# Performance work log

Hardware: AMD Instinct MI355X
Metric: run time of the kernel (lower is better)

Reference implementation:

```python
import jax, jax.numpy as jnp
import numpy as np

B, W, CBLK, C, H, L, VOCAB = 8, 512, 24, 512, 8, 2, 256
HD = C // H


def _ln(x, g, b, eps=1e-5):
    m = x.mean(-1, keepdims=True)
    v = ((x - m) ** 2).mean(-1, keepdims=True)
    return (x - m) * jax.lax.rsqrt(v + eps) * g + b


def _causal_attn(q, k, v):
    # q,k,v: [..., T, hd]; causal softmax attention, scale 1/sqrt(hd)
    T = q.shape[-2]
    scale = 1.0 / (q.shape[-1] ** 0.5)
    s = jnp.einsum('...qd,...kd->...qk', q, k) * scale
    mask = jnp.tril(jnp.ones((T, T), dtype=bool))
    s = jnp.where(mask, s, jnp.finfo(s.dtype).min)
    return jnp.einsum('...qk,...kd->...qd', jax.nn.softmax(s, axis=-1), v)


def _mha_char(seq, w_qkv, last_ix):
    # seq: [B,W,c,C]; per-word causal char attention, then gather row last_ix
    b, w, c, _ = seq.shape
    q, k, v = jnp.split(seq @ w_qkv, 3, axis=-1)
    sh = lambda t: t.reshape(b, w, c, H, HD).transpose(0, 1, 3, 2, 4)
    o = _causal_attn(sh(q), sh(k), sh(v))          # [B,W,H,c,hd]
    o = o.transpose(0, 1, 3, 2, 4).reshape(b, w, c, C)
    return jnp.take_along_axis(o, last_ix[:, :, None, None], axis=2)[:, :, 0, :]


def _mha_word(x, w_qkv, w_proj):
    b, w, _ = x.shape
    q, k, v = jnp.split(x @ w_qkv, 3, axis=-1)
    sh = lambda t: t.reshape(b, w, H, HD).transpose(0, 2, 1, 3)
    o = _causal_attn(sh(q), sh(k), sh(v))
    o = o.transpose(0, 2, 1, 3).reshape(b, w, C)
    return o @ w_proj


def setup_inputs() -> dict:
    key = jax.random.key(0)
    ks = jax.random.split(key, 16)
    # ragged word lengths in [1, CBLK]; mask = ones then zeros (as produced by pad())
    lengths = jax.random.randint(ks[0], (B, W), 1, CBLK + 1)
    attention_mask = (jnp.arange(CBLK)[None, None, :] < lengths[:, :, None]).astype(jnp.int32)
    x = jax.random.randint(ks[1], (B, W, CBLK), 0, VOCAB).astype(jnp.int32)
    std = 0.02
    res_std = std * (2 * L) ** -0.5  # res_flag init scaling
    n = lambda k, s, sd=std: sd * jax.random.normal(k, s, dtype=jnp.float32)
    return dict(
        x=x, attention_mask=attention_mask,
        cte=n(ks[2], (VOCAB, C)), cpe=n(ks[3], (CBLK, C)), wpe=n(ks[4], (W, C)),
        ln1_g=jnp.ones((L, C)), ln1_b=jnp.zeros((L, C)),
        ln2_g=jnp.ones((L, C)), ln2_b=jnp.zeros((L, C)),
        ln3_g=jnp.ones((L, C)), ln3_b=jnp.zeros((L, C)),
        cattn_w=n(ks[5], (L, C, 3 * C)), cattn_proj=n(ks[6], (L, C, C)),
        wattn_w=n(ks[7], (L, C, 3 * C)), wattn_proj=n(ks[8], (L, C, C), res_std),
        mlp_fc=n(ks[9], (L, C, 4 * C)), mlp_proj=n(ks[10], (L, 4 * C, C), res_std),
        proj_w=n(ks[11], (C, CBLK * C)), lm_head_w=n(ks[12], (C, VOCAB)),
    )


def reference(x, attention_mask, cte, cpe, wpe, ln1_g, ln1_b, ln2_g, ln2_b, ln3_g, ln3_b,
              cattn_w, cattn_proj, wattn_w, wattn_proj, mlp_fc, mlp_proj, proj_w, lm_head_w):
    last_ix = attention_mask.sum(axis=2) - 1           # [B,W], last real char per word
    state = cte[x] + cpe[None, None, :, :]             # [B,W,c,C]
    context = None                                     # current_conv.context/pad, vectorized
    for l in range(L):
        if l == 0:
            # first_time: operate on full padded char sequences, cache ln_1 output
            hln = _ln(state, ln1_g[l], ln1_b[l])       # [B,W,c,C]
            context = hln
            seq = hln
        else:
            # splice the new word vector into position last_ix of the cached context
            hln = _ln(state, ln1_g[l], ln1_b[l])       # [B,W,C]
            repl = jnp.arange(CBLK)[None, None, :] == last_ix[:, :, None]
            seq = jnp.where(repl[..., None], hln[:, :, None, :], context)
        o = _mha_char(seq, cattn_w[l], last_ix)        # [B,W,C]
        if l == 0:
            o = o + wpe[None, :, :]                    # word pos emb added only first_time
        state = o @ cattn_proj[l]                      # note: no residual around c_attn
        state = state + _mha_word(_ln(state, ln2_g[l], ln2_b[l]), wattn_w[l], wattn_proj[l])
        hm = _ln(state, ln3_g[l], ln3_b[l])
        state = state + jax.nn.gelu(hm @ mlp_fc[l], approximate=False) @ mlp_proj[l]
    y = (state @ proj_w).reshape(B, W, CBLK, C)
    return y @ lm_head_w                               # logits [B,W,CBLK,VOCAB]
```

## Files before the change

kernel.cpp:

```cpp
#include <hip/hip_runtime.h>
#include <hip/hip_bf16.h>
#include <math.h>


namespace {

constexpr int Bn = 8, Wn = 512, CB = 24, Cd = 512, Hn = 8, Lln = 2, Vn = 256, HDn = 64;
constexpr int BW = Bn * Wn;
constexpr int C3 = 3 * Cd;
constexpr int FF = 4 * Cd;
constexpr int NROW = BW * CB;

typedef unsigned short u16;
typedef short short8 __attribute__((ext_vector_type(8)));
typedef float f32x4 __attribute__((ext_vector_type(4)));
typedef __attribute__((address_space(1))) void gvoid_t;
typedef __attribute__((address_space(3))) void lvoid_t;

__device__ __forceinline__ u16 f2bu(float f) {
  __hip_bfloat16 h = __float2bfloat16(f);
  return __builtin_bit_cast(u16, h);
}
__device__ __forceinline__ float bu2f(u16 u) {
  return __bfloat162float(__builtin_bit_cast(__hip_bfloat16, u));
}
__device__ __forceinline__ float geluf(float x) {
  return 0.5f * x * (1.0f + erff(x * 0.7071067811865475f));
}
__device__ __forceinline__ void gl16(const void* g, void* l) {
  __builtin_amdgcn_global_load_lds((gvoid_t*)g, (lvoid_t*)l, 16, 0, 0);
}

__global__ void k_lastix(const int* __restrict__ mask, int* __restrict__ lastix) {
  int i = blockIdx.x * 256 + threadIdx.x;
  if (i < BW) {
    int s = 0;
#pragma unroll
    for (int j = 0; j < CB; ++j) s += mask[i * CB + j];
    lastix[i] = s - 1;
  }
}

__device__ __forceinline__ void f2b8(const float* __restrict__ s, u16* __restrict__ d) {
  float4 a = *(const float4*)s;
  float4 b = *(const float4*)(s + 4);
  union { uint4 u; u16 h[8]; } pk;
  pk.h[0] = f2bu(a.x); pk.h[1] = f2bu(a.y); pk.h[2] = f2bu(a.z); pk.h[3] = f2bu(a.w);
  pk.h[4] = f2bu(b.x); pk.h[5] = f2bu(b.y); pk.h[6] = f2bu(b.z); pk.h[7] = f2bu(b.w);
  *(uint4*)d = pk.u;
}

__device__ __forceinline__ void wT_tile(const float* __restrict__ src, u16* __restrict__ dst,
                                        int K, int N, int n0, int k0,
                                        u16 T[64][72], int tid) {
  int kl = tid >> 2, nc = (tid & 3) * 16;
  const float* s = src + (long)(k0 + kl) * N + n0 + nc;
#pragma unroll
  for (int u = 0; u < 4; ++u) {
    float4 f = *(const float4*)(s + u * 4);
    T[nc + u * 4 + 0][kl] = f2bu(f.x);
    T[nc + u * 4 + 1][kl] = f2bu(f.y);
    T[nc + u * 4 + 2][kl] = f2bu(f.z);
    T[nc + u * 4 + 3][kl] = f2bu(f.w);
  }
  __syncthreads();
  int nl = tid >> 2, kc = (tid & 3) * 16;
  u16* d = dst + (long)(n0 + nl) * K + k0 + kc;
  *(uint4*)d = *(uint4*)&T[nl][kc];
  *(uint4*)(d + 8) = *(uint4*)&T[nl][kc + 8];
}

__global__ __launch_bounds__(256) void k_prep(
    const float* __restrict__ proj_w, u16* __restrict__ projwb,
    const float* __restrict__ cattn_w, u16* __restrict__ wcb,
    const float* __restrict__ lm_head, u16* __restrict__ lmhT,
    const float* __restrict__ cattn_proj, const float* __restrict__ wattn_w,
    const float* __restrict__ wattn_proj, const float* __restrict__ mlp_fc,
    const float* __restrict__ mlp_proj, u16* __restrict__ wT) {
  __shared__ u16 T[64][72];
  int b = blockIdx.x, tid = threadIdx.x;
  if (b < 3072) { long i = ((long)b * 256 + tid) * 8; f2b8(proj_w + i, projwb + i); return; }
  b -= 3072;
  if (b < 768) { long i = ((long)b * 256 + tid) * 8; f2b8(cattn_w + i, wcb + i); return; }
  b -= 768;
  if (b < 32) { wT_tile(lm_head, lmhT, Cd, Vn, (b & 3) * 64, (b >> 2) * 64, T, tid); return; }
  b -= 32;
  int l = b >> 10, r = b & 1023;
  size_t lw = (size_t)(2 * C3 * Cd + 2 * Cd * Cd + 2 * FF * Cd);
  u16* bl = wT + l * lw;
  const float* src; u16* dst; int K, N, nt;
  if (r < 192)      { src = cattn_w + (size_t)l * Cd * C3;    dst = bl;                              K = Cd; N = C3; nt = 24; }
  else if (r < 256) { src = cattn_proj + (size_t)l * Cd * Cd; dst = bl + C3 * Cd;                    K = Cd; N = Cd; nt = 8;  r -= 192; }
  else if (r < 448) { src = wattn_w + (size_t)l * Cd * C3;    dst = bl + C3 * Cd + Cd * Cd;          K = Cd; N = C3; nt = 24; r -= 256; }
  else if (r < 512) { src = wattn_proj + (size_t)l * Cd * Cd; dst = bl + 2 * C3 * Cd + Cd * Cd;      K = Cd; N = Cd; nt = 8;  r -= 448; }
  else if (r < 768) { src = mlp_fc + (size_t)l * Cd * FF;     dst = bl + 2 * C3 * Cd + 2 * Cd * Cd;  K = Cd; N = FF; nt = 32; r -= 512; }
  else              { src = mlp_proj + (size_t)l * FF * Cd;   dst = bl + 2 * C3 * Cd + 2 * Cd * Cd + FF * Cd; K = FF; N = Cd; nt = 8; r -= 768; }
  wT_tile(src, dst, K, N, (r % nt) * 64, (r / nt) * 64, T, tid);
}

__global__ __launch_bounds__(64) void k_embed_ln(
    const int* __restrict__ x, const float* __restrict__ cte, const float* __restrict__ cpe,
    const float* __restrict__ g, const float* __restrict__ b,
    const int* __restrict__ lastix, u16* __restrict__ ctx) {
  int r = blockIdx.x;
  int bw = r / CB, ch = r - bw * CB;
  if (ch > lastix[bw]) return;
  int tok = x[r];
  const float* e = cte + (long)tok * Cd;
  const float* pe = cpe + (long)ch * Cd;
  int lane = threadIdx.x;
  float v[8];
  float s = 0.f, sq = 0.f;
#pragma unroll
  for (int u = 0; u < 2; ++u) {
    float4 a = *(const float4*)(e + u * 256 + lane * 4);
    float4 p4 = *(const float4*)(pe + u * 256 + lane * 4);
    v[u * 4 + 0] = a.x + p4.x; v[u * 4 + 1] = a.y + p4.y;
    v[u * 4 + 2] = a.z + p4.z; v[u * 4 + 3] = a.w + p4.w;
  }
#pragma unroll
  for (int u = 0; u < 8; ++u) { s += v[u]; sq += v[u] * v[u]; }
#pragma unroll
  for (int m = 32; m; m >>= 1) { s += __shfl_xor(s, m); sq += __shfl_xor(sq, m); }
  float mean = s * (1.0f / Cd);
  float var = sq * (1.0f / Cd) - mean * mean;
  float rs = rsqrtf(var + 1e-5f);
  u16* o = ctx + (long)r * Cd;
#pragma unroll
  for (int u = 0; u < 2; ++u) {
    int c0 = u * 256 + lane * 4;
    float4 g4 = *(const float4*)(g + c0);
    float4 b4 = *(const float4*)(b + c0);
    float o0 = (v[u * 4 + 0] - mean) * rs * g4.x + b4.x;
    float o1 = (v[u * 4 + 1] - mean) * rs * g4.y + b4.y;
    float o2 = (v[u * 4 + 2] - mean) * rs * g4.z + b4.z;
    float o3 = (v[u * 4 + 3] - mean) * rs * g4.w + b4.w;
    uint2 w;
    w.x = (unsigned)f2bu(o0) | ((unsigned)f2bu(o1) << 16);
    w.y = (unsigned)f2bu(o2) | ((unsigned)f2bu(o3) << 16);
    *(uint2*)(o + c0) = w;
  }
}

__global__ __launch_bounds__(64) void k_ln(
    const float* __restrict__ X, u16* __restrict__ Y,
    const float* __restrict__ g, const float* __restrict__ b) {
  long r = blockIdx.x;
  const float* xr = X + r * Cd;
  int lane = threadIdx.x;
  float v[8];
  float s = 0.f, sq = 0.f;
#pragma unroll
  for (int u = 0; u < 2; ++u) {
    float4 a = *(const float4*)(xr + u * 256 + lane * 4);
    v[u * 4 + 0] = a.x; v[u * 4 + 1] = a.y; v[u * 4 + 2] = a.z; v[u * 4 + 3] = a.w;
  }
#pragma unroll
  for (int u = 0; u < 8; ++u) { s += v[u]; sq += v[u] * v[u]; }
#pragma unroll
  for (int m = 32; m; m >>= 1) { s += __shfl_xor(s, m); sq += __shfl_xor(sq, m); }
  float mean = s * (1.0f / Cd);
  float var = sq * (1.0f / Cd) - mean * mean;
  float rs = rsqrtf(var + 1e-5f);
  u16* o = Y + r * Cd;
#pragma unroll
  for (int u = 0; u < 2; ++u) {
    int c0 = u * 256 + lane * 4;
    float4 g4 = *(const float4*)(g + c0);
    float4 b4 = *(const float4*)(b + c0);
    float o0 = (v[u * 4 + 0] - mean) * rs * g4.x + b4.x;
    float o1 = (v[u * 4 + 1] - mean) * rs * g4.y + b4.y;
    float o2 = (v[u * 4 + 2] - mean) * rs * g4.z + b4.z;
    float o3 = (v[u * 4 + 3] - mean) * rs * g4.w + b4.w;
    uint2 w;
    w.x = (unsigned)f2bu(o0) | ((unsigned)f2bu(o1) << 16);
    w.y = (unsigned)f2bu(o2) | ((unsigned)f2bu(o3) << 16);
    *(uint2*)(o + c0) = w;
  }
}

__global__ __launch_bounds__(64) void k_gather_last(
    const u16* __restrict__ ctx, const int* __restrict__ lastix, u16* __restrict__ qin) {
  long bw = blockIdx.x;
  int r = (int)bw * CB + lastix[bw];
  const uint4* s = (const uint4*)(ctx + (long)r * Cd);
  uint4* d = (uint4*)(qin + bw * Cd);
  d[threadIdx.x] = s[threadIdx.x];
}

template <int BM, int BN, int EPI, int OUTBF>
__global__ __launch_bounds__(256) void k_mgemm(
    const u16* __restrict__ A, int lda, long sA1, long sA2,
    const u16* __restrict__ Bt, int ldb, long sB1, long sB2,
    void* __restrict__ Cv, int ldc, long sC1, long sC2,
    const float* __restrict__ R, u16* __restrict__ D2,
    const float* __restrict__ PL, const u16* __restrict__ VL,
    const float* __restrict__ WP, int K, int zdiv) {
  constexpr int WM = BM / 2;
  constexpr int WN = BN / 2;
  constexpr int FM = WM / 16, FN = WN / 16;
  __shared__ u16 As[BM * 32];
  __shared__ u16 Bs[BN * 32];
  long m0 = (long)blockIdx.y * BM, n0 = (long)blockIdx.x * BN;
  int z = blockIdx.z;
  int z1 = z / zdiv, z2 = z - z1 * zdiv;
  A += z1 * sA1 + z2 * sA2;
  Bt += z1 * sB1 + z2 * sB2;
  long coff = z1 * sC1 + z2 * sC2;
  int tid = threadIdx.x;
  int wid = tid >> 6, lane = tid & 63;
  int wr = wid >> 1, wc = wid & 1;

  const int srow = tid >> 2, skk = (tid & 3) * 8;
  const u16* Ald[BM / 64];
  const u16* Bld[BN / 64];
#pragma unroll
  for (int i = 0; i < BM / 64; ++i) Ald[i] = A + (m0 + srow + i * 64) * (long)lda + skk;
#pragma unroll
  for (int i = 0; i < BN / 64; ++i) Bld[i] = Bt + (n0 + srow + i * 64) * (long)ldb + skk;

  f32x4 acc[FM][FN] = {};
  const int fr = lane & 15, kg = lane >> 4;

  for (int k0 = 0; k0 < K; k0 += 32) {
#pragma unroll
    for (int i = 0; i < BM / 64; ++i) gl16(Ald[i] + k0, &As[(tid + i * 256) * 8]);
#pragma unroll
    for (int i = 0; i < BN / 64; ++i) gl16(Bld[i] + k0, &Bs[(tid + i * 256) * 8]);
    __syncthreads();
    short8 af[FM], bf[FN];
#pragma unroll
    for (int m = 0; m < FM; ++m)
      af[m] = *(const short8*)&As[(wr * WM + m * 16 + fr) * 32 + kg * 8];
#pragma unroll
    for (int n = 0; n < FN; ++n)
      bf[n] = *(const short8*)&Bs[(wc * WN + n * 16 + fr) * 32 + kg * 8];
#pragma unroll
    for (int m = 0; m < FM; ++m)
#pragma unroll
      for (int n = 0; n < FN; ++n)
        acc[m][n] = __builtin_amdgcn_mfma_f32_16x16x32_bf16(af[m], bf[n], acc[m][n], 0, 0, 0);
    __syncthreads();
  }
  int ccol = lane & 15, crow4 = (lane >> 4) * 4;
#pragma unroll
  for (int m = 0; m < FM; ++m)
#pragma unroll
    for (int n = 0; n < FN; ++n)
#pragma unroll
      for (int q = 0; q < 4; ++q) {
        long gr = m0 + wr * WM + m * 16 + crow4 + q;
        long gc = n0 + wc * WN + n * 16 + ccol;
        float v = acc[m][n][q];
        long idx = gr * (long)ldc + gc + coff;
        if (EPI == 1 || EPI == 3) v += R[idx];
        if (EPI == 2) v = geluf(v);
        if (EPI == 4) {
          v += PL[gr * 8 + z2] * bu2f(VL[gr * (long)C3 + 2 * Cd + z2 * 64 + gc]);
          if (WP) v += WP[(long)(gr & (Wn - 1)) * Cd + z2 * 64 + gc];
        }
        if (EPI == 3) {
          ((float*)Cv)[idx] = v;
          D2[idx] = f2bu(v);
        } else if (OUTBF) {
          ((u16*)Cv)[idx] = f2bu(v);
        } else {
          ((float*)Cv)[idx] = v;
        }
      }
}

__global__ __launch_bounds__(256) void k_cattn2(
    const u16* __restrict__ ctx, const u16* __restrict__ qtil,
    const u16* __restrict__ qkvc, const int* __restrict__ lastix,
    u16* __restrict__ U, float* __restrict__ plast) {
  int gw = blockIdx.x;
  int li = lastix[gw];
  __shared__ u16 ctxs[CB][512];
  __shared__ u16 qks[2][512];
  __shared__ float sp[Hn][CB];
  int tid = threadIdx.x;
  for (int u = tid; u < li * 64; u += 256) {
    int row = u >> 6, c = (u & 63) * 8;
    *(uint4*)&ctxs[row][c] = *(const uint4*)(ctx + ((long)(gw * CB + row)) * Cd + c);
  }
  if (tid < 128) {
    int row = tid >> 6, c = (tid & 63) * 8;
    *(uint4*)&qks[row][c] = *(const uint4*)(qkvc + (long)gw * C3 + row * 512 + c);
  }
  int wid = tid >> 6, lane = tid & 63;
  int h0 = wid * 2, h1 = h0 + 1;
  float q0[8], q1[8];
  {
    const u16* q0p = qtil + (long)gw * 4096 + h0 * 512 + lane * 8;
    uint4 a = *(const uint4*)q0p;
    uint4 b = *(const uint4*)(q0p + 512);
    const u16* qa = (const u16*)&a;
    const u16* qb = (const u16*)&b;
#pragma unroll
    for (int u = 0; u < 8; ++u) { q0[u] = bu2f(qa[u]); q1[u] = bu2f(qb[u]); }
  }
  __syncthreads();
  for (int j = 0; j < li; ++j) {
    float p0 = 0.f, p1 = 0.f;
    const u16* cv = &ctxs[j][lane * 8];
#pragma unroll
    for (int u = 0; u < 8; ++u) {
      float c = bu2f(cv[u]);
      p0 += c * q0[u];
      p1 += c * q1[u];
    }
#pragma unroll
    for (int m = 32; m; m >>= 1) { p0 += __shfl_xor(p0, m); p1 += __shfl_xor(p1, m); }
    if (lane == 0) { sp[h0][j] = p0 * 0.125f; sp[h1][j] = p1 * 0.125f; }
  }
  {
    float pr = 0.f;
    const u16* qq = &qks[0][lane * 8];
    const u16* kk = &qks[1][lane * 8];
#pragma unroll
    for (int u = 0; u < 8; ++u) pr += bu2f(qq[u]) * bu2f(kk[u]);
    float a0 = ((lane >> 3) == h0) ? pr : 0.f;
    float a1 = ((lane >> 3) == h1) ? pr : 0.f;
#pragma unroll
    for (int m = 32; m; m >>= 1) { a0 += __shfl_xor(a0, m); a1 += __shfl_xor(a1, m); }
    if (lane == 0) { sp[h0][li] = a0 * 0.125f; sp[h1][li] = a1 * 0.125f; }
  }
  __syncthreads();
  if (tid < 8) {
    float m = -3.4e38f;
    for (int j = 0; j <= li; ++j) m = fmaxf(m, sp[tid][j]);
    float s = 0.f;
    for (int j = 0; j <= li; ++j) { float e = expf(sp[tid][j] - m); sp[tid][j] = e; s += e; }
    float inv = 1.0f / s;
    for (int j = 0; j <= li; ++j) sp[tid][j] *= inv;
    plast[gw * 8 + tid] = sp[tid][li];
  }
  __syncthreads();
  int h = tid >> 5, d0 = (tid & 31) * 16;
  float uacc[16];
#pragma unroll
  for (int i = 0; i < 16; ++i) uacc[i] = 0.f;
  for (int j = 0; j < li; ++j) {
    float p = sp[h][j];
    const u16* cv = &ctxs[j][d0];
#pragma unroll
    for (int i = 0; i < 16; ++i) uacc[i] += p * bu2f(cv[i]);
  }
  union { uint4 q[2]; u16 hh[16]; } pk;
#pragma unroll
  for (int i = 0; i < 16; ++i) pk.hh[i] = f2bu(uacc[i]);
  u16* d = U + (long)gw * 4096 + h * 512 + d0;
  *(uint4*)d = pk.q[0];
  *(uint4*)(d + 8) = pk.q[1];
}

__global__ __launch_bounds__(256) void k_vt(const u16* __restrict__ qkv, u16* __restrict__ Vt) {
  __shared__ u16 T[64][72];
  int z = blockIdx.y, jt = blockIdx.x;
  int b = z >> 3, h = z & 7;
  int tid = threadIdx.x;
  int jl = tid >> 2, dc = (tid & 3) * 16;
  const u16* s = qkv + ((long)(b * Wn + jt * 64 + jl)) * C3 + 2 * Cd + h * HDn + dc;
  *(uint4*)&T[jl][dc] = *(const uint4*)s;
  *(uint4*)&T[jl][dc + 8] = *(const uint4*)(s + 8);
  __syncthreads();
  int dl = tid >> 2, jc = (tid & 3) * 16;
  u16 tmp[16];
#pragma unroll
  for (int u = 0; u < 16; ++u) tmp[u] = T[jc + u][dl];
  u16* d = Vt + (long)z * HDn * Wn + (long)dl * Wn + jt * 64 + jc;
  *(uint4*)d = *(uint4*)&tmp[0];
  *(uint4*)(d + 8) = *(uint4*)&tmp[8];
}

__global__ __launch_bounds__(64) void k_wsoftmax(const float* __restrict__ S,
                                                 u16* __restrict__ P) {
  long row = blockIdx.x;
  int i = (int)(row & (Wn - 1));
  const float* p = S + row * Wn;
  int lane = threadIdx.x;
  int j0 = lane * 8;
  float v[8];
  float4 a = *(const float4*)(p + j0);
  float4 b4 = *(const float4*)(p + j0 + 4);
  v[0] = a.x; v[1] = a.y; v[2] = a.z; v[3] = a.w;
  v[4] = b4.x; v[5] = b4.y; v[6] = b4.z; v[7] = b4.w;
  float m = -3.4e38f;
#pragma unroll
  for (int u = 0; u < 8; ++u) {
    v[u] = (j0 + u <= i) ? v[u] * 0.125f : -3.4e38f;
    m = fmaxf(m, v[u]);
  }
#pragma unroll
  for (int mk = 32; mk; mk >>= 1) m = fmaxf(m, __shfl_xor(m, mk));
  float s = 0.f;
#pragma unroll
  for (int u = 0; u < 8; ++u) {
    float e = (j0 + u <= i) ? expf(v[u] - m) : 0.f;
    v[u] = e; s += e;
  }
#pragma unroll
  for (int mk = 32; mk; mk >>= 1) s += __shfl_xor(s, mk);
  float inv = 1.0f / s;
  union { uint4 u; u16 h[8]; } pk;
#pragma unroll
  for (int u = 0; u < 8; ++u) pk.h[u] = f2bu(v[u] * inv);
  *(uint4*)(P + row * Wn + j0) = pk.u;
}

template <int BM, int BN, int EPI, int OUTBF>
static inline void mgemm(hipStream_t st,
    const u16* A, int lda, long sA1, long sA2,
    const u16* Bt, int ldb, long sB1, long sB2,
    void* C, int ldc, long sC1, long sC2,
    const float* R, int M, int N, int K, int nz, int zdiv,
    u16* D2 = nullptr, const float* PL = nullptr, const u16* VL = nullptr,
    const float* WP = nullptr) {
  dim3 g(N / BN, (M + BM - 1) / BM, nz);
  hipLaunchKernelGGL((k_mgemm<BM, BN, EPI, OUTBF>), g, dim3(256), 0, st,
                     A, lda, sA1, sA2, Bt, ldb, sB1, sB2, C, ldc, sC1, sC2,
                     R ? R : (const float*)C, D2, PL, VL, WP, K, zdiv);
}

}

extern "C" void kernel_launch(void* const* d_in, const int* in_sizes, int n_in,
                              void* d_out, int out_size, void* d_ws, size_t ws_size,
                              hipStream_t stream) {
  (void)in_sizes; (void)n_in; (void)out_size; (void)ws_size;
  const int*   x          = (const int*)d_in[0];
  const int*   amask      = (const int*)d_in[1];
  const float* cte        = (const float*)d_in[2];
  const float* cpe        = (const float*)d_in[3];
  const float* wpe        = (const float*)d_in[4];
  const float* ln1g       = (const float*)d_in[5];
  const float* ln1b       = (const float*)d_in[6];
  const float* ln2g       = (const float*)d_in[7];
  const float* ln2b       = (const float*)d_in[8];
  const float* ln3g       = (const float*)d_in[9];
  const float* ln3b       = (const float*)d_in[10];
  const float* cattn_w    = (const float*)d_in[11];
  const float* cattn_proj = (const float*)d_in[12];
  const float* wattn_w    = (const float*)d_in[13];
  const float* wattn_proj = (const float*)d_in[14];
  const float* mlp_fc     = (const float*)d_in[15];
  const float* mlp_proj   = (const float*)d_in[16];
  const float* proj_w     = (const float*)d_in[17];
  const float* lm_head    = (const float*)d_in[18];
  float* out = (float*)d_out;

  char* base = (char*)d_ws;
  size_t off = 0;
  auto alloc = [&](size_t bytes) -> char* {
    char* r = base + off;
    off += (bytes + 255) & ~(size_t)255;
    return r;
  };
  int*   lastix = (int*)alloc((size_t)BW * 4);
  float* plast  = (float*)alloc((size_t)BW * 8 * 4);
  u16*   ctx    = (u16*)alloc((size_t)NROW * Cd * 2);
  char*  big    = alloc((size_t)105 * 1024 * 1024);
  u16*   kvq    = (u16*)alloc((size_t)BW * C3 * 2);
  u16*   qin    = (u16*)alloc((size_t)BW * Cd * 2);
  float* state  = (float*)alloc((size_t)BW * Cd * 4);
  u16*   stateb = (u16*)alloc((size_t)BW * Cd * 2);
  u16*   hln    = (u16*)alloc((size_t)BW * Cd * 2);
  u16*   ao     = (u16*)alloc((size_t)BW * Cd * 2);
  u16*   wT     = (u16*)alloc((size_t)2 * (2 * C3 * Cd + 2 * Cd * Cd + 2 * FF * Cd) * 2);
  u16*   wcb    = (u16*)alloc((size_t)2 * Cd * C3 * 2);
  u16*   projwb = (u16*)alloc((size_t)Cd * CB * Cd * 2);
  u16*   lmhT   = (u16*)alloc((size_t)Vn * Cd * 2);

  u16*   U     = (u16*)big;
  u16*   qtil  = (u16*)(big + (size_t)35651584);
  float* S     = (float*)big;
  u16*   P     = (u16*)(big + (size_t)67108864);
  u16*   Vt    = (u16*)(big + (size_t)100663296);
  u16*   mlph  = (u16*)big;
  u16*   combT = (u16*)big;

  size_t lw = (size_t)(2 * C3 * Cd + 2 * Cd * Cd + 2 * FF * Cd);
  auto cwT    = [&](int l) { return wT + l * lw; };
  auto cprojT = [&](int l) { return wT + l * lw + C3 * Cd; };
  auto wwT    = [&](int l) { return wT + l * lw + C3 * Cd + Cd * Cd; };
  auto wprojT = [&](int l) { return wT + l * lw + 2 * C3 * Cd + Cd * Cd; };
  auto fcT    = [&](int l) { return wT + l * lw + 2 * C3 * Cd + 2 * Cd * Cd; };
  auto mprojT = [&](int l) { return wT + l * lw + 2 * C3 * Cd + 2 * Cd * Cd + FF * Cd; };

  hipLaunchKernelGGL(k_lastix, dim3(16), dim3(256), 0, stream, amask, lastix);
  hipLaunchKernelGGL(k_prep, dim3(5920), dim3(256), 0, stream,
                     proj_w, projwb, cattn_w, wcb, lm_head, lmhT,
                     cattn_proj, wattn_w, wattn_proj, mlp_fc, mlp_proj, wT);
  hipLaunchKernelGGL(k_embed_ln, dim3(NROW), dim3(64), 0, stream,
                     x, cte, cpe, ln1g, ln1b, lastix, ctx);

  for (int l = 0; l < Lln; ++l) {
    u16* qkvc = kvq;
    u16* qkvw = kvq;
    if (l == 0)
      hipLaunchKernelGGL(k_gather_last, dim3(BW), dim3(64), 0, stream, ctx, lastix, qin);
    else
      hipLaunchKernelGGL(k_ln, dim3(BW), dim3(64), 0, stream, state, qin, ln1g + Cd, ln1b + Cd);
    mgemm<128, 64, 0, 1>(stream, qin, Cd, 0, 0, cwT(l), Cd, 0, 0,
                         qkvc, C3, 0, 0, nullptr, BW, C3, Cd, 1, 1);
    mgemm<64, 64, 0, 1>(stream, qkvc, C3, 0, 64,
                        wcb + (size_t)l * Cd * C3 + Cd, C3, 0, 64,
                        qtil, 8 * Cd, 0, Cd, nullptr, BW, Cd, HDn, 8, 8);
    hipLaunchKernelGGL(k_cattn2, dim3(BW), dim3(256), 0, stream,
                       ctx, qtil, qkvc, lastix, U, plast);
    mgemm<64, 64, 4, 1>(stream, U, 8 * Cd, 0, Cd,
                        cwT(l) + (size_t)(2 * Cd) * Cd, Cd, 0, (long)HDn * Cd,
                        ao, Cd, 0, HDn, nullptr, BW, HDn, Cd, 8, 8,
                        nullptr, plast, qkvc, l == 0 ? wpe : nullptr);
    mgemm<64, 64, 0, 0>(stream, ao, Cd, 0, 0, cprojT(l), Cd, 0, 0,
                        state, Cd, 0, 0, nullptr, BW, Cd, Cd, 1, 1);
    hipLaunchKernelGGL(k_ln, dim3(BW), dim3(64), 0, stream, state, hln, ln2g + l * Cd, ln2b + l * Cd);
    mgemm<128, 64, 0, 1>(stream, hln, Cd, 0, 0, wwT(l), Cd, 0, 0,
                         qkvw, C3, 0, 0, nullptr, BW, C3, Cd, 1, 1);
    mgemm<128, 128, 0, 0>(stream, qkvw, C3, (long)Wn * C3, HDn,
                          qkvw + Cd, C3, (long)Wn * C3, HDn,
                          S, Wn, (long)8 * Wn * Wn, (long)Wn * Wn,
                          nullptr, Wn, Wn, HDn, 64, 8);
    hipLaunchKernelGGL(k_vt, dim3(Wn / 64, 64), dim3(256), 0, stream, qkvw, Vt);
    hipLaunchKernelGGL(k_wsoftmax, dim3(64 * Wn), dim3(64), 0, stream, S, P);
    mgemm<64, 64, 0, 1>(stream, P, Wn, (long)8 * Wn * Wn, (long)Wn * Wn,
                        Vt, Wn, (long)8 * HDn * Wn, (long)HDn * Wn,
                        ao, Cd, (long)Wn * Cd, HDn,
                        nullptr, Wn, HDn, Wn, 64, 8);
    mgemm<64, 64, 1, 0>(stream, ao, Cd, 0, 0, wprojT(l), Cd, 0, 0,
                        state, Cd, 0, 0, state, BW, Cd, Cd, 1, 1);
    hipLaunchKernelGGL(k_ln, dim3(BW), dim3(64), 0, stream, state, hln, ln3g + l * Cd, ln3b + l * Cd);
    mgemm<128, 128, 2, 1>(stream, hln, Cd, 0, 0, fcT(l), Cd, 0, 0,
                          mlph, FF, 0, 0, nullptr, BW, FF, Cd, 1, 1);
    mgemm<64, 64, 3, 0>(stream, mlph, FF, 0, 0, mprojT(l), FF, 0, 0,
                        state, Cd, 0, 0, state, BW, Cd, FF, 1, 1, stateb);
  }

  mgemm<64, 64, 0, 1>(stream, lmhT, Cd, 0, 0,
                      projwb, CB * Cd, 0, Cd,
                      combT, Cd, 0, (long)Vn * Cd,
                      nullptr, Vn, Cd, Cd, CB, CB);
  mgemm<128, 128, 0, 0>(stream, stateb, Cd, 0, 0, combT, Cd, 0, 0,
                        out, CB * Vn, 0, 0, nullptr, BW, CB * Vn, Cd, 1, 1);
}
```

Measured before the change: 623.8 us.

## Fuse word attention into a flash-style MFMA kernel with causal tile skipping

```diff
diff --git a/kernel.cpp b/kernel.cpp
--- a/kernel.cpp
+++ b/kernel.cpp
@@ -301,7 +301,29 @@
     for (int u = 0; u < 8; ++u) { q0[u] = bu2f(qa[u]); q1[u] = bu2f(qb[u]); }
   }
   __syncthreads();
-  for (int j = 0; j < li; ++j) {
+  int j = 0;
+  for (; j + 2 <= li; j += 2) {
+    float p0a = 0.f, p1a = 0.f, p0b = 0.f, p1b = 0.f;
+    const u16* cva = &ctxs[j][lane * 8];
+    const u16* cvb = &ctxs[j + 1][lane * 8];
+#pragma unroll
+    for (int u = 0; u < 8; ++u) {
+      float ca = bu2f(cva[u]);
+      float cb = bu2f(cvb[u]);
+      p0a += ca * q0[u]; p1a += ca * q1[u];
+      p0b += cb * q0[u]; p1b += cb * q1[u];
+    }
+#pragma unroll
+    for (int m = 32; m; m >>= 1) {
+      p0a += __shfl_xor(p0a, m); p1a += __shfl_xor(p1a, m);
+      p0b += __shfl_xor(p0b, m); p1b += __shfl_xor(p1b, m);
+    }
+    if (lane == 0) {
+      sp[h0][j] = p0a * 0.125f; sp[h1][j] = p1a * 0.125f;
+      sp[h0][j + 1] = p0b * 0.125f; sp[h1][j + 1] = p1b * 0.125f;
+    }
+  }
+  if (j < li) {
     float p0 = 0.f, p1 = 0.f;
     const u16* cv = &ctxs[j][lane * 8];
 #pragma unroll
@@ -329,11 +351,11 @@
   __syncthreads();
   if (tid < 8) {
     float m = -3.4e38f;
-    for (int j = 0; j <= li; ++j) m = fmaxf(m, sp[tid][j]);
+    for (int jj = 0; jj <= li; ++jj) m = fmaxf(m, sp[tid][jj]);
     float s = 0.f;
-    for (int j = 0; j <= li; ++j) { float e = expf(sp[tid][j] - m); sp[tid][j] = e; s += e; }
+    for (int jj = 0; jj <= li; ++jj) { float e = expf(sp[tid][jj] - m); sp[tid][jj] = e; s += e; }
     float inv = 1.0f / s;
-    for (int j = 0; j <= li; ++j) sp[tid][j] *= inv;
+    for (int jj = 0; jj <= li; ++jj) sp[tid][jj] *= inv;
     plast[gw * 8 + tid] = sp[tid][li];
   }
   __syncthreads();
@@ -341,9 +363,9 @@
   float uacc[16];
 #pragma unroll
   for (int i = 0; i < 16; ++i) uacc[i] = 0.f;
-  for (int j = 0; j < li; ++j) {
-    float p = sp[h][j];
-    const u16* cv = &ctxs[j][d0];
+  for (int jj = 0; jj < li; ++jj) {
+    float p = sp[h][jj];
+    const u16* cv = &ctxs[jj][d0];
 #pragma unroll
     for (int i = 0; i < 16; ++i) uacc[i] += p * bu2f(cv[i]);
   }
@@ -374,39 +396,113 @@
   *(uint4*)(d + 8) = *(uint4*)&tmp[8];
 }
 
-__global__ __launch_bounds__(64) void k_wsoftmax(const float* __restrict__ S,
-                                                 u16* __restrict__ P) {
-  long row = blockIdx.x;
-  int i = (int)(row & (Wn - 1));
-  const float* p = S + row * Wn;
-  int lane = threadIdx.x;
-  int j0 = lane * 8;
-  float v[8];
-  float4 a = *(const float4*)(p + j0);
-  float4 b4 = *(const float4*)(p + j0 + 4);
-  v[0] = a.x; v[1] = a.y; v[2] = a.z; v[3] = a.w;
-  v[4] = b4.x; v[5] = b4.y; v[6] = b4.z; v[7] = b4.w;
-  float m = -3.4e38f;
-#pragma unroll
-  for (int u = 0; u < 8; ++u) {
-    v[u] = (j0 + u <= i) ? v[u] * 0.125f : -3.4e38f;
-    m = fmaxf(m, v[u]);
-  }
-#pragma unroll
-  for (int mk = 32; mk; mk >>= 1) m = fmaxf(m, __shfl_xor(m, mk));
-  float s = 0.f;
-#pragma unroll
-  for (int u = 0; u < 8; ++u) {
-    float e = (j0 + u <= i) ? expf(v[u] - m) : 0.f;
-    v[u] = e; s += e;
-  }
-#pragma unroll
-  for (int mk = 32; mk; mk >>= 1) s += __shfl_xor(s, mk);
-  float inv = 1.0f / s;
-  union { uint4 u; u16 h[8]; } pk;
-#pragma unroll
-  for (int u = 0; u < 8; ++u) pk.h[u] = f2bu(v[u] * inv);
-  *(uint4*)(P + row * Wn + j0) = pk.u;
+__global__ __launch_bounds__(256) void k_fattn(
+    const u16* __restrict__ qkv, const u16* __restrict__ Vt, u16* __restrict__ ao) {
+  constexpr int ST = 68;
+  __shared__ u16 Ks[64 * ST];
+  __shared__ u16 Vs[64 * ST];
+  __shared__ u16 Ps[4][16 * ST];
+  int qt = blockIdx.x;
+  int z  = blockIdx.y;
+  int b = z >> 3, h = z & 7;
+  int tid = threadIdx.x;
+  int w = tid >> 6, lane = tid & 63;
+  int fr = lane & 15, kg = lane >> 4;
+
+  short8 qf[2];
+  {
+    const u16* qp = qkv + ((long)(b * Wn + qt * 64 + w * 16 + fr)) * C3 + h * 64 + kg * 8;
+    qf[0] = *(const short8*)qp;
+    qf[1] = *(const short8*)(qp + 32);
+  }
+  f32x4 oacc[4] = {};
+  float mrow[4], lrow[4];
+#pragma unroll
+  for (int q = 0; q < 4; ++q) { mrow[q] = -3.4e38f; lrow[q] = 0.f; }
+
+  for (int kt = 0; kt <= qt; ++kt) {
+    __syncthreads();
+    {
+      int r = tid >> 2, c = (tid & 3) * 16;
+      const u16* kp = qkv + ((long)(b * Wn + kt * 64 + r)) * C3 + Cd + h * 64 + c;
+      *(uint4*)&Ks[r * ST + c] = *(const uint4*)kp;
+      *(uint4*)&Ks[r * ST + c + 8] = *(const uint4*)(kp + 8);
+      const u16* vp = Vt + (long)z * (64 * Wn) + (long)r * Wn + kt * 64 + c;
+      *(uint4*)&Vs[r * ST + c] = *(const uint4*)vp;
+      *(uint4*)&Vs[r * ST + c + 8] = *(const uint4*)(vp + 8);
+    }
+    __syncthreads();
+    f32x4 s[4];
+#pragma unroll
+    for (int n = 0; n < 4; ++n) {
+      short8 kf0 = *(const short8*)&Ks[(n * 16 + fr) * ST + kg * 8];
+      short8 kf1 = *(const short8*)&Ks[(n * 16 + fr) * ST + kg * 8 + 32];
+      f32x4 a = {};
+      a = __builtin_amdgcn_mfma_f32_16x16x32_bf16(qf[0], kf0, a, 0, 0, 0);
+      a = __builtin_amdgcn_mfma_f32_16x16x32_bf16(qf[1], kf1, a, 0, 0, 0);
+      s[n] = a;
+    }
+    int irow0 = qt * 64 + w * 16 + kg * 4;
+#pragma unroll
+    for (int n = 0; n < 4; ++n) {
+      int jcol = kt * 64 + n * 16 + fr;
+#pragma unroll
+      for (int q = 0; q < 4; ++q) {
+        float v = s[n][q] * 0.125f;
+        s[n][q] = (jcol > irow0 + q) ? -3.4e38f : v;
+      }
+    }
+    float sf[4];
+#pragma unroll
+    for (int q = 0; q < 4; ++q) {
+      float mm = fmaxf(fmaxf(s[0][q], s[1][q]), fmaxf(s[2][q], s[3][q]));
+      mm = fmaxf(mm, __shfl_xor(mm, 1));
+      mm = fmaxf(mm, __shfl_xor(mm, 2));
+      mm = fmaxf(mm, __shfl_xor(mm, 4));
+      mm = fmaxf(mm, __shfl_xor(mm, 8));
+      float mnew = fmaxf(mrow[q], mm);
+      sf[q] = expf(mrow[q] - mnew);
+      mrow[q] = mnew;
+    }
+    float ls[4] = {0.f, 0.f, 0.f, 0.f};
+#pragma unroll
+    for (int n = 0; n < 4; ++n) {
+#pragma unroll
+      for (int q = 0; q < 4; ++q) {
+        float p = expf(s[n][q] - mrow[q]);
+        u16 pb = f2bu(p);
+        ls[q] += bu2f(pb);
+        Ps[w][(kg * 4 + q) * ST + n * 16 + fr] = pb;
+      }
+    }
+#pragma unroll
+    for (int q = 0; q < 4; ++q) {
+      float l = ls[q];
+      l += __shfl_xor(l, 1); l += __shfl_xor(l, 2);
+      l += __shfl_xor(l, 4); l += __shfl_xor(l, 8);
+      lrow[q] = lrow[q] * sf[q] + l;
+#pragma unroll
+      for (int n = 0; n < 4; ++n) oacc[n][q] *= sf[q];
+    }
+    asm volatile("s_waitcnt lgkmcnt(0)" ::: "memory");
+    short8 pa0 = *(const short8*)&Ps[w][fr * ST + kg * 8];
+    short8 pa1 = *(const short8*)&Ps[w][fr * ST + kg * 8 + 32];
+#pragma unroll
+    for (int n = 0; n < 4; ++n) {
+      short8 vf0 = *(const short8*)&Vs[(n * 16 + fr) * ST + kg * 8];
+      short8 vf1 = *(const short8*)&Vs[(n * 16 + fr) * ST + kg * 8 + 32];
+      oacc[n] = __builtin_amdgcn_mfma_f32_16x16x32_bf16(pa0, vf0, oacc[n], 0, 0, 0);
+      oacc[n] = __builtin_amdgcn_mfma_f32_16x16x32_bf16(pa1, vf1, oacc[n], 0, 0, 0);
+    }
+  }
+  int orow = b * Wn + qt * 64 + w * 16 + kg * 4;
+#pragma unroll
+  for (int q = 0; q < 4; ++q) {
+    float inv = 1.0f / lrow[q];
+#pragma unroll
+    for (int n = 0; n < 4; ++n)
+      ao[(long)(orow + q) * Cd + h * 64 + n * 16 + fr] = f2bu(oacc[n][q] * inv);
+  }
 }
 
 template <int BM, int BN, int EPI, int OUTBF>
@@ -474,9 +570,7 @@
 
   u16*   U     = (u16*)big;
   u16*   qtil  = (u16*)(big + (size_t)35651584);
-  float* S     = (float*)big;
-  u16*   P     = (u16*)(big + (size_t)67108864);
-  u16*   Vt    = (u16*)(big + (size_t)100663296);
+  u16*   Vt    = (u16*)(big + (size_t)71303168);
   u16*   mlph  = (u16*)big;
   u16*   combT = (u16*)big;
 
@@ -518,16 +612,8 @@
     hipLaunchKernelGGL(k_ln, dim3(BW), dim3(64), 0, stream, state, hln, ln2g + l * Cd, ln2b + l * Cd);
     mgemm<128, 64, 0, 1>(stream, hln, Cd, 0, 0, wwT(l), Cd, 0, 0,
                          qkvw, C3, 0, 0, nullptr, BW, C3, Cd, 1, 1);
-    mgemm<128, 128, 0, 0>(stream, qkvw, C3, (long)Wn * C3, HDn,
-                          qkvw + Cd, C3, (long)Wn * C3, HDn,
-                          S, Wn, (long)8 * Wn * Wn, (long)Wn * Wn,
-                          nullptr, Wn, Wn, HDn, 64, 8);
     hipLaunchKernelGGL(k_vt, dim3(Wn / 64, 64), dim3(256), 0, stream, qkvw, Vt);
-    hipLaunchKernelGGL(k_wsoftmax, dim3(64 * Wn), dim3(64), 0, stream, S, P);
-    mgemm<64, 64, 0, 1>(stream, P, Wn, (long)8 * Wn * Wn, (long)Wn * Wn,
-                        Vt, Wn, (long)8 * HDn * Wn, (long)HDn * Wn,
-                        ao, Cd, (long)Wn * Cd, HDn,
-                        nullptr, Wn, HDn, Wn, 64, 8);
+    hipLaunchKernelGGL(k_fattn, dim3(8, 64), dim3(256), 0, stream, qkvw, Vt, ao);
     mgemm<64, 64, 1, 0>(stream, ao, Cd, 0, 0, wprojT(l), Cd, 0, 0,
                         state, Cd, 0, 0, state, BW, Cd, Cd, 1, 1);
     hipLaunchKernelGGL(k_ln, dim3(BW), dim3(64), 0, stream, state, hln, ln3g + l * Cd, ln3b + l * Cd);
```

Result: faster. 578.8 us (-7.2%).
